# Kernel optimization log

Hardware: AMD Instinct MI355X
Metric: run time of the kernel (lower is better)

Reference implementation:

```python
import jax, jax.numpy as jnp
import numpy as np

D_MODEL = 1024
N_HEADS = 16
D_K = D_MODEL // N_HEADS  # 64
D_V = D_MODEL // N_HEADS  # 64
B, S = 2, 2048


def setup_inputs() -> dict:
    key = jax.random.key(0)
    ks = jax.random.split(key, 8)
    inp = {
        "Q": jax.random.normal(ks[0], (B, S, D_MODEL), dtype=jnp.float32),
        "K": jax.random.normal(ks[1], (B, S, D_MODEL), dtype=jnp.float32),
        "V": jax.random.normal(ks[2], (B, S, D_MODEL), dtype=jnp.float32),
        "prev": jax.random.normal(ks[3], (B, N_HEADS, S, S), dtype=jnp.float32) * 0.1,
        # torch nn.Linear weights are [out_features, in_features]
        "W_Q": jax.random.normal(ks[4], (N_HEADS * D_K, D_MODEL), dtype=jnp.float32) / np.sqrt(D_MODEL),
        "W_K": jax.random.normal(ks[5], (N_HEADS * D_K, D_MODEL), dtype=jnp.float32) / np.sqrt(D_MODEL),
        "W_V": jax.random.normal(ks[6], (N_HEADS * D_V, D_MODEL), dtype=jnp.float32) / np.sqrt(D_MODEL),
        "W_O": jax.random.normal(ks[7], (D_MODEL, N_HEADS * D_V), dtype=jnp.float32) / np.sqrt(N_HEADS * D_V),
    }
    return inp


def reference(Q, K, V, prev, W_Q, W_K, W_V, W_O):
    scale = D_K ** (-0.5)
    # projections: x @ W.T, then split heads -> (b, h, s, d)
    q = jnp.einsum('bsm,em->bse', Q, W_Q).reshape(B, S, N_HEADS, D_K).transpose(0, 2, 1, 3)
    k = jnp.einsum('bsm,em->bse', K, W_K).reshape(B, S, N_HEADS, D_K).transpose(0, 2, 1, 3)
    v = jnp.einsum('bsm,em->bse', V, W_V).reshape(B, S, N_HEADS, D_V).transpose(0, 2, 1, 3)
    scores = jnp.einsum('bhqd,bhkd->bhqk', q, k) * scale + prev
    attn = jax.nn.softmax(scores, axis=-1)  # attn_dropout = 0 (eval)
    context = jnp.einsum('bhqk,bhkd->bhqd', attn, v)
    context = context.transpose(0, 2, 1, 3).reshape(B, S, N_HEADS * D_V)
    output = jnp.einsum('bse,me->bsm', context, W_O)  # proj_dropout = 0 (eval)
    return (output, attn, scores)
```

## Files before the change

### kernel.cpp

```cpp
#include <hip/hip_runtime.h>

#define S_LEN 2048
#define NH 16
#define DH 64
#define DM 1024
#define NB 2
#define BS 4096

typedef __attribute__((ext_vector_type(4))) float f32x4;
typedef __attribute__((ext_vector_type(8))) short bfrag;

__device__ __forceinline__ unsigned short f2bf(float f) {
    unsigned u = __builtin_bit_cast(unsigned, f);
    u += 0x7FFFu + ((u >> 16) & 1u);
    return (unsigned short)(u >> 16);
}

__global__ __launch_bounds__(256) void cast_kernel(const float* __restrict__ in,
                                                   unsigned short* __restrict__ out, int n4) {
    int i = blockIdx.x * 256 + threadIdx.x;
    if (i < n4) {
        float4 v = reinterpret_cast<const float4*>(in)[i];
        ushort4 o;
        o.x = f2bf(v.x); o.y = f2bf(v.y); o.z = f2bf(v.z); o.w = f2bf(v.w);
        reinterpret_cast<ushort4*>(out)[i] = o;
    }
}

template <int EPI>
__global__ __launch_bounds__(256) void gemm_bt(const unsigned short* __restrict__ A,
                                               const unsigned short* __restrict__ Bt,
                                               void* __restrict__ Out, int M, int N, int K) {
    const int tid = threadIdx.x;
    const int lane = tid & 63;
    const int w = tid >> 6, wr = w >> 1, wc = w & 1;
    const int m0 = blockIdx.y * 128;
    const int n0 = blockIdx.x * 128;

    __shared__ unsigned short sA[128 * 64];
    __shared__ unsigned short sB[128 * 64];

    f32x4 acc[4][4];
#pragma unroll
    for (int i = 0; i < 4; ++i)
#pragma unroll
        for (int j = 0; j < 4; ++j) acc[i][j] = (f32x4){0.f, 0.f, 0.f, 0.f};

    for (int k0 = 0; k0 < K; k0 += 64) {
#pragma unroll
        for (int i = 0; i < 4; ++i) {
            int c = i * 256 + tid;
            int row = c >> 3, col8 = c & 7;
            int swz = (col8 * 8) ^ ((row & 7) * 8);
            *reinterpret_cast<int4*>(sA + row * 64 + swz) =
                *reinterpret_cast<const int4*>(A + (size_t)(m0 + row) * K + k0 + col8 * 8);
            *reinterpret_cast<int4*>(sB + row * 64 + swz) =
                *reinterpret_cast<const int4*>(Bt + (size_t)(n0 + row) * K + k0 + col8 * 8);
        }
        __syncthreads();
#pragma unroll
        for (int kk = 0; kk < 2; ++kk) {
            bfrag a[4], b[4];
#pragma unroll
            for (int f = 0; f < 4; ++f) {
                int ra = wr * 64 + f * 16 + (lane & 15);
                a[f] = *reinterpret_cast<const bfrag*>(
                    sA + ra * 64 + ((kk * 32 + (lane >> 4) * 8) ^ ((ra & 7) * 8)));
                int rb = wc * 64 + f * 16 + (lane & 15);
                b[f] = *reinterpret_cast<const bfrag*>(
                    sB + rb * 64 + ((kk * 32 + (lane >> 4) * 8) ^ ((rb & 7) * 8)));
            }
#pragma unroll
            for (int fm = 0; fm < 4; ++fm)
#pragma unroll
                for (int fn = 0; fn < 4; ++fn)
                    acc[fm][fn] =
                        __builtin_amdgcn_mfma_f32_16x16x32_bf16(a[fm], b[fn], acc[fm][fn], 0, 0, 0);
        }
        __syncthreads();
    }

    if constexpr (EPI == 1) {
#pragma unroll
        for (int fm = 0; fm < 4; ++fm)
#pragma unroll
            for (int fn = 0; fn < 4; ++fn) {
                int sbase = m0 + wr * 64 + fm * 16 + ((lane >> 4) << 2);
                int gcol = n0 + wc * 64 + fn * 16 + (lane & 15);
                int b = sbase >> 11, s = sbase & 2047, h = gcol >> 6, d = gcol & 63;
                ushort4 o;
                o.x = f2bf(acc[fm][fn][0]); o.y = f2bf(acc[fm][fn][1]);
                o.z = f2bf(acc[fm][fn][2]); o.w = f2bf(acc[fm][fn][3]);
                *reinterpret_cast<ushort4*>((unsigned short*)Out +
                                            ((size_t)(b * NH + h) * DH + d) * S_LEN + s) = o;
            }
    } else {
#pragma unroll
        for (int fm = 0; fm < 4; ++fm)
#pragma unroll
            for (int fn = 0; fn < 4; ++fn)
#pragma unroll
                for (int r = 0; r < 4; ++r) {
                    int grow = m0 + wr * 64 + fm * 16 + ((lane >> 4) << 2) + r;
                    int gcol = n0 + wc * 64 + fn * 16 + (lane & 15);
                    float v = acc[fm][fn][r];
                    if constexpr (EPI == 0) {
                        int b = grow >> 11, s = grow & 2047, h = gcol >> 6, d = gcol & 63;
                        ((unsigned short*)Out)[((size_t)(b * NH + h) * S_LEN + s) * DH + d] =
                            f2bf(v);
                    } else {
                        ((float*)Out)[(size_t)grow * N + gcol] = v;
                    }
                }
    }
}

__global__ __launch_bounds__(256) void scores_kernel(const unsigned short* __restrict__ qh,
                                                     const unsigned short* __restrict__ kh,
                                                     const float* __restrict__ prev,
                                                     float* __restrict__ scores) {
    const int z = blockIdx.z;
    const int tid = threadIdx.x;
    const int lane = tid & 63;
    const int w = tid >> 6, wr = w >> 1, wc = w & 1;
    const int m0 = blockIdx.y * 128, n0 = blockIdx.x * 128;
    const unsigned short* A = qh + (size_t)z * S_LEN * DH;
    const unsigned short* Bt = kh + (size_t)z * S_LEN * DH;

    __shared__ unsigned short sA[128 * 64];
    __shared__ unsigned short sB[128 * 64];

#pragma unroll
    for (int i = 0; i < 4; ++i) {
        int c = i * 256 + tid;
        int row = c >> 3, col8 = c & 7;
        int swz = (col8 * 8) ^ ((row & 7) * 8);
        *reinterpret_cast<int4*>(sA + row * 64 + swz) =
            *reinterpret_cast<const int4*>(A + (size_t)(m0 + row) * DH + col8 * 8);
        *reinterpret_cast<int4*>(sB + row * 64 + swz) =
            *reinterpret_cast<const int4*>(Bt + (size_t)(n0 + row) * DH + col8 * 8);
    }
    __syncthreads();

    f32x4 acc[4][4];
#pragma unroll
    for (int i = 0; i < 4; ++i)
#pragma unroll
        for (int j = 0; j < 4; ++j) acc[i][j] = (f32x4){0.f, 0.f, 0.f, 0.f};

#pragma unroll
    for (int kk = 0; kk < 2; ++kk) {
        bfrag a[4], b[4];
#pragma unroll
        for (int f = 0; f < 4; ++f) {
            int ra = wr * 64 + f * 16 + (lane & 15);
            a[f] = *reinterpret_cast<const bfrag*>(
                sA + ra * 64 + ((kk * 32 + (lane >> 4) * 8) ^ ((ra & 7) * 8)));
            int rb = wc * 64 + f * 16 + (lane & 15);
            b[f] = *reinterpret_cast<const bfrag*>(
                sB + rb * 64 + ((kk * 32 + (lane >> 4) * 8) ^ ((rb & 7) * 8)));
        }
#pragma unroll
        for (int fm = 0; fm < 4; ++fm)
#pragma unroll
            for (int fn = 0; fn < 4; ++fn)
                acc[fm][fn] =
                    __builtin_amdgcn_mfma_f32_16x16x32_bf16(a[fm], b[fn], acc[fm][fn], 0, 0, 0);
    }

    const float scale = 0.125f;
#pragma unroll
    for (int fm = 0; fm < 4; ++fm)
#pragma unroll
        for (int fn = 0; fn < 4; ++fn)
#pragma unroll
            for (int r = 0; r < 4; ++r) {
                int grow = m0 + wr * 64 + fm * 16 + ((lane >> 4) << 2) + r;
                int gcol = n0 + wc * 64 + fn * 16 + (lane & 15);
                size_t idx = (size_t)z * S_LEN * S_LEN + (size_t)grow * S_LEN + gcol;
                scores[idx] = acc[fm][fn][r] * scale + prev[idx];
            }
}

__global__ __launch_bounds__(256) void softmax_kernel(const float* __restrict__ scores,
                                                      float* __restrict__ attn) {
    const size_t row = (size_t)blockIdx.x * 4 + (threadIdx.x >> 6);
    const int lane = threadIdx.x & 63;
    const float* rp = scores + row * S_LEN;
    float4 v[8];
    float m = -1e30f;
#pragma unroll
    for (int it = 0; it < 8; ++it) {
        v[it] = *reinterpret_cast<const float4*>(rp + (it * 64 + lane) * 4);
        m = fmaxf(m, fmaxf(fmaxf(v[it].x, v[it].y), fmaxf(v[it].z, v[it].w)));
    }
#pragma unroll
    for (int s = 32; s >= 1; s >>= 1) m = fmaxf(m, __shfl_xor(m, s));
    float sum = 0.f;
#pragma unroll
    for (int it = 0; it < 8; ++it) {
        v[it].x = __expf(v[it].x - m); v[it].y = __expf(v[it].y - m);
        v[it].z = __expf(v[it].z - m); v[it].w = __expf(v[it].w - m);
        sum += v[it].x + v[it].y + v[it].z + v[it].w;
    }
#pragma unroll
    for (int s = 32; s >= 1; s >>= 1) sum += __shfl_xor(sum, s);
    const float inv = 1.0f / sum;
    float* op = attn + row * S_LEN;
#pragma unroll
    for (int it = 0; it < 8; ++it) {
        float4 o = make_float4(v[it].x * inv, v[it].y * inv, v[it].z * inv, v[it].w * inv);
        *reinterpret_cast<float4*>(op + (it * 64 + lane) * 4) = o;
    }
}

__global__ __launch_bounds__(256) void pv_kernel(const float* __restrict__ attn,
                                                 const unsigned short* __restrict__ vT,
                                                 unsigned short* __restrict__ ctx) {
    const int z = blockIdx.z;
    const int tid = threadIdx.x, lane = tid & 63;
    const int w = tid >> 6, wr = w >> 1, wc = w & 1;
    const int m0 = blockIdx.x * 128;
    const float* Az = attn + (size_t)z * S_LEN * S_LEN;
    const unsigned short* Bz = vT + (size_t)z * DH * S_LEN;

    __shared__ unsigned short sA[128 * 64];
    __shared__ unsigned short sB[64 * 64];

    f32x4 acc[4][2];
#pragma unroll
    for (int i = 0; i < 4; ++i)
#pragma unroll
        for (int j = 0; j < 2; ++j) acc[i][j] = (f32x4){0.f, 0.f, 0.f, 0.f};

    for (int k0 = 0; k0 < S_LEN; k0 += 64) {
#pragma unroll
        for (int i = 0; i < 8; ++i) {
            int c = i * 256 + tid;
            int row = c >> 4, col4 = c & 15;
            float4 v = *reinterpret_cast<const float4*>(Az + (size_t)(m0 + row) * S_LEN + k0 +
                                                        col4 * 4);
            ushort4 o;
            o.x = f2bf(v.x); o.y = f2bf(v.y); o.z = f2bf(v.z); o.w = f2bf(v.w);
            *reinterpret_cast<ushort4*>(sA + row * 64 + ((col4 * 4) ^ ((row & 7) * 8))) = o;
        }
#pragma unroll
        for (int i = 0; i < 2; ++i) {
            int c = i * 256 + tid;
            int row = c >> 3, col8 = c & 7;
            *reinterpret_cast<int4*>(sB + row * 64 + ((col8 * 8) ^ ((row & 7) * 8))) =
                *reinterpret_cast<const int4*>(Bz + (size_t)row * S_LEN + k0 + col8 * 8);
        }
        __syncthreads();
#pragma unroll
        for (int kk = 0; kk < 2; ++kk) {
            bfrag a[4], b[2];
#pragma unroll
            for (int f = 0; f < 4; ++f) {
                int ra = wr * 64 + f * 16 + (lane & 15);
                a[f] = *reinterpret_cast<const bfrag*>(
                    sA + ra * 64 + ((kk * 32 + (lane >> 4) * 8) ^ ((ra & 7) * 8)));
            }
#pragma unroll
            for (int f = 0; f < 2; ++f) {
                int rb = wc * 32 + f * 16 + (lane & 15);
                b[f] = *reinterpret_cast<const bfrag*>(
                    sB + rb * 64 + ((kk * 32 + (lane >> 4) * 8) ^ ((rb & 7) * 8)));
            }
#pragma unroll
            for (int fm = 0; fm < 4; ++fm)
#pragma unroll
                for (int fn = 0; fn < 2; ++fn)
                    acc[fm][fn] =
                        __builtin_amdgcn_mfma_f32_16x16x32_bf16(a[fm], b[fn], acc[fm][fn], 0, 0, 0);
        }
        __syncthreads();
    }

    const int b = z >> 4, h = z & 15;
#pragma unroll
    for (int fm = 0; fm < 4; ++fm)
#pragma unroll
        for (int fn = 0; fn < 2; ++fn)
#pragma unroll
            for (int r = 0; r < 4; ++r) {
                int s = m0 + wr * 64 + fm * 16 + ((lane >> 4) << 2) + r;
                int d = wc * 32 + fn * 16 + (lane & 15);
                ctx[((size_t)(b * S_LEN + s)) * DM + h * DH + d] = f2bf(acc[fm][fn][r]);
            }
}

extern "C" void kernel_launch(void* const* d_in, const int* in_sizes, int n_in, void* d_out,
                              int out_size, void* d_ws, size_t ws_size, hipStream_t stream) {
    const float* Q = (const float*)d_in[0];
    const float* K = (const float*)d_in[1];
    const float* V = (const float*)d_in[2];
    const float* prev = (const float*)d_in[3];
    const float* Wq = (const float*)d_in[4];
    const float* Wk = (const float*)d_in[5];
    const float* Wv = (const float*)d_in[6];
    const float* Wo = (const float*)d_in[7];

    float* out = (float*)d_out;
    float* attn = out + (size_t)BS * DM;
    float* scores = attn + (size_t)NB * NH * S_LEN * S_LEN;

    unsigned short* ws = (unsigned short*)d_ws;
    unsigned short* Qc = ws;
    unsigned short* Kc = Qc + (size_t)BS * DM;
    unsigned short* Vc = Kc + (size_t)BS * DM;
    unsigned short* Wqc = Vc + (size_t)BS * DM;
    unsigned short* Wkc = Wqc + (size_t)DM * DM;
    unsigned short* Wvc = Wkc + (size_t)DM * DM;
    unsigned short* Woc = Wvc + (size_t)DM * DM;
    unsigned short* qh = Woc + (size_t)DM * DM;
    unsigned short* kh = qh + (size_t)BS * DM;
    unsigned short* vT = kh + (size_t)BS * DM;
    unsigned short* ctx = vT + (size_t)BS * DM;

    cast_kernel<<<BS * DM / 4 / 256, 256, 0, stream>>>(Q, Qc, BS * DM / 4);
    cast_kernel<<<BS * DM / 4 / 256, 256, 0, stream>>>(K, Kc, BS * DM / 4);
    cast_kernel<<<BS * DM / 4 / 256, 256, 0, stream>>>(V, Vc, BS * DM / 4);
    cast_kernel<<<DM * DM / 4 / 256, 256, 0, stream>>>(Wq, Wqc, DM * DM / 4);
    cast_kernel<<<DM * DM / 4 / 256, 256, 0, stream>>>(Wk, Wkc, DM * DM / 4);
    cast_kernel<<<DM * DM / 4 / 256, 256, 0, stream>>>(Wv, Wvc, DM * DM / 4);
    cast_kernel<<<DM * DM / 4 / 256, 256, 0, stream>>>(Wo, Woc, DM * DM / 4);

    dim3 gp(DM / 128, BS / 128, 1);
    gemm_bt<0><<<gp, 256, 0, stream>>>(Qc, Wqc, qh, BS, DM, DM);
    gemm_bt<0><<<gp, 256, 0, stream>>>(Kc, Wkc, kh, BS, DM, DM);
    gemm_bt<1><<<gp, 256, 0, stream>>>(Vc, Wvc, vT, BS, DM, DM);

    dim3 gs(S_LEN / 128, S_LEN / 128, NB * NH);
    scores_kernel<<<gs, 256, 0, stream>>>(qh, kh, prev, scores);

    softmax_kernel<<<NB * NH * S_LEN / 4, 256, 0, stream>>>(scores, attn);

    dim3 gv(S_LEN / 128, 1, NB * NH);
    pv_kernel<<<gv, 256, 0, stream>>>(attn, vT, ctx);

    gemm_bt<2><<<gp, 256, 0, stream>>>(ctx, Woc, out, BS, DM, DM);
}
```

Before: 706.4 us.

## Fuse attention into single two-pass kernel and cast fp32 inputs inside GEMM loads

Replaces the separate scores, softmax and PV kernels with one fused kernel per 128-row query tile. Its first pass computes QK^T plus prev, writes scores and keeps running max and sum. Its second pass rereads scores, writes attn, and feeds bf16 P through shared memory into the PV MFMA. The standalone cast kernels are removed, and the GEMMs now convert fp32 inputs and weights to bf16 while staging tiles into LDS. This aims to cut the full-matrix attn reread by the PV kernel, the separate softmax pass, and several launches. The trade-off is that the fused grid has only 512 blocks with serialized per-block loops, and every GEMM block now repeats the weight conversion.

```diff
diff --git a/kernel.cpp b/kernel.cpp
--- a/kernel.cpp
+++ b/kernel.cpp
@@ -16,20 +16,9 @@
     return (unsigned short)(u >> 16);
 }
 
-__global__ __launch_bounds__(256) void cast_kernel(const float* __restrict__ in,
-                                                   unsigned short* __restrict__ out, int n4) {
-    int i = blockIdx.x * 256 + threadIdx.x;
-    if (i < n4) {
-        float4 v = reinterpret_cast<const float4*>(in)[i];
-        ushort4 o;
-        o.x = f2bf(v.x); o.y = f2bf(v.y); o.z = f2bf(v.z); o.w = f2bf(v.w);
-        reinterpret_cast<ushort4*>(out)[i] = o;
-    }
-}
-
-template <int EPI>
-__global__ __launch_bounds__(256) void gemm_bt(const unsigned short* __restrict__ A,
-                                               const unsigned short* __restrict__ Bt,
+template <int EPI, int AF, int BF>
+__global__ __launch_bounds__(256) void gemm_bt(const void* __restrict__ Av,
+                                               const void* __restrict__ Bv,
                                                void* __restrict__ Out, int M, int N, int K) {
     const int tid = threadIdx.x;
     const int lane = tid & 63;
@@ -47,15 +36,49 @@
         for (int j = 0; j < 4; ++j) acc[i][j] = (f32x4){0.f, 0.f, 0.f, 0.f};
 
     for (int k0 = 0; k0 < K; k0 += 64) {
-#pragma unroll
-        for (int i = 0; i < 4; ++i) {
-            int c = i * 256 + tid;
-            int row = c >> 3, col8 = c & 7;
-            int swz = (col8 * 8) ^ ((row & 7) * 8);
-            *reinterpret_cast<int4*>(sA + row * 64 + swz) =
-                *reinterpret_cast<const int4*>(A + (size_t)(m0 + row) * K + k0 + col8 * 8);
-            *reinterpret_cast<int4*>(sB + row * 64 + swz) =
-                *reinterpret_cast<const int4*>(Bt + (size_t)(n0 + row) * K + k0 + col8 * 8);
+        if constexpr (AF) {
+            const float* A = (const float*)Av;
+#pragma unroll
+            for (int i = 0; i < 8; ++i) {
+                int c = i * 256 + tid;
+                int row = c >> 4, col4 = c & 15;
+                float4 v = *reinterpret_cast<const float4*>(A + (size_t)(m0 + row) * K + k0 +
+                                                            col4 * 4);
+                ushort4 o;
+                o.x = f2bf(v.x); o.y = f2bf(v.y); o.z = f2bf(v.z); o.w = f2bf(v.w);
+                *reinterpret_cast<ushort4*>(sA + row * 64 + ((col4 * 4) ^ ((row & 7) * 8))) = o;
+            }
+        } else {
+            const unsigned short* A = (const unsigned short*)Av;
+#pragma unroll
+            for (int i = 0; i < 4; ++i) {
+                int c = i * 256 + tid;
+                int row = c >> 3, col8 = c & 7;
+                *reinterpret_cast<int4*>(sA + row * 64 + ((col8 * 8) ^ ((row & 7) * 8))) =
+                    *reinterpret_cast<const int4*>(A + (size_t)(m0 + row) * K + k0 + col8 * 8);
+            }
+        }
+        if constexpr (BF) {
+            const float* B = (const float*)Bv;
+#pragma unroll
+            for (int i = 0; i < 8; ++i) {
+                int c = i * 256 + tid;
+                int row = c >> 4, col4 = c & 15;
+                float4 v = *reinterpret_cast<const float4*>(B + (size_t)(n0 + row) * K + k0 +
+                                                            col4 * 4);
+                ushort4 o;
+                o.x = f2bf(v.x); o.y = f2bf(v.y); o.z = f2bf(v.z); o.w = f2bf(v.w);
+                *reinterpret_cast<ushort4*>(sB + row * 64 + ((col4 * 4) ^ ((row & 7) * 8))) = o;
+            }
+        } else {
+            const unsigned short* B = (const unsigned short*)Bv;
+#pragma unroll
+            for (int i = 0; i < 4; ++i) {
+                int c = i * 256 + tid;
+                int row = c >> 3, col8 = c & 7;
+                *reinterpret_cast<int4*>(sB + row * 64 + ((col8 * 8) ^ ((row & 7) * 8))) =
+                    *reinterpret_cast<const int4*>(B + (size_t)(n0 + row) * K + k0 + col8 * 8);
+            }
         }
         __syncthreads();
 #pragma unroll
@@ -115,178 +138,196 @@
     }
 }
 
-__global__ __launch_bounds__(256) void scores_kernel(const unsigned short* __restrict__ qh,
-                                                     const unsigned short* __restrict__ kh,
-                                                     const float* __restrict__ prev,
-                                                     float* __restrict__ scores) {
+__global__ __launch_bounds__(256) void attn_fused(const unsigned short* __restrict__ qh,
+                                                  const unsigned short* __restrict__ kh,
+                                                  const unsigned short* __restrict__ vT,
+                                                  const float* __restrict__ prev,
+                                                  float* __restrict__ scores,
+                                                  float* __restrict__ attn,
+                                                  unsigned short* __restrict__ ctx) {
     const int z = blockIdx.z;
+    const int m0 = blockIdx.x * 128;
     const int tid = threadIdx.x;
     const int lane = tid & 63;
-    const int w = tid >> 6, wr = w >> 1, wc = w & 1;
-    const int m0 = blockIdx.y * 128, n0 = blockIdx.x * 128;
-    const unsigned short* A = qh + (size_t)z * S_LEN * DH;
-    const unsigned short* Bt = kh + (size_t)z * S_LEN * DH;
-
-    __shared__ unsigned short sA[128 * 64];
-    __shared__ unsigned short sB[128 * 64];
+    const int w = tid >> 6;
+
+    __shared__ unsigned short sQ[128 * 64];
+    __shared__ unsigned short sKV[128 * 64];
+    __shared__ unsigned short sP[128 * 128];
+
+    const unsigned short* Qz = qh + (size_t)z * S_LEN * DH;
+    const unsigned short* Kz = kh + (size_t)z * S_LEN * DH;
+    const unsigned short* Vz = vT + (size_t)z * DH * S_LEN;
+    const size_t zbase = (size_t)z * S_LEN * S_LEN;
 
 #pragma unroll
     for (int i = 0; i < 4; ++i) {
         int c = i * 256 + tid;
         int row = c >> 3, col8 = c & 7;
-        int swz = (col8 * 8) ^ ((row & 7) * 8);
-        *reinterpret_cast<int4*>(sA + row * 64 + swz) =
-            *reinterpret_cast<const int4*>(A + (size_t)(m0 + row) * DH + col8 * 8);
-        *reinterpret_cast<int4*>(sB + row * 64 + swz) =
-            *reinterpret_cast<const int4*>(Bt + (size_t)(n0 + row) * DH + col8 * 8);
-    }
-    __syncthreads();
-
-    f32x4 acc[4][4];
-#pragma unroll
-    for (int i = 0; i < 4; ++i)
-#pragma unroll
-        for (int j = 0; j < 4; ++j) acc[i][j] = (f32x4){0.f, 0.f, 0.f, 0.f};
-
-#pragma unroll
-    for (int kk = 0; kk < 2; ++kk) {
-        bfrag a[4], b[4];
-#pragma unroll
-        for (int f = 0; f < 4; ++f) {
-            int ra = wr * 64 + f * 16 + (lane & 15);
-            a[f] = *reinterpret_cast<const bfrag*>(
-                sA + ra * 64 + ((kk * 32 + (lane >> 4) * 8) ^ ((ra & 7) * 8)));
-            int rb = wc * 64 + f * 16 + (lane & 15);
-            b[f] = *reinterpret_cast<const bfrag*>(
-                sB + rb * 64 + ((kk * 32 + (lane >> 4) * 8) ^ ((rb & 7) * 8)));
-        }
-#pragma unroll
-        for (int fm = 0; fm < 4; ++fm)
-#pragma unroll
-            for (int fn = 0; fn < 4; ++fn)
-                acc[fm][fn] =
-                    __builtin_amdgcn_mfma_f32_16x16x32_bf16(a[fm], b[fn], acc[fm][fn], 0, 0, 0);
-    }
+        *reinterpret_cast<int4*>(sQ + row * 64 + ((col8 * 8) ^ ((row & 7) * 8))) =
+            *reinterpret_cast<const int4*>(Qz + (size_t)(m0 + row) * DH + col8 * 8);
+    }
+
+    float m_r[2][4], l_r[2][4];
+#pragma unroll
+    for (int fm = 0; fm < 2; ++fm)
+#pragma unroll
+        for (int r = 0; r < 4; ++r) { m_r[fm][r] = -1e30f; l_r[fm][r] = 0.f; }
 
     const float scale = 0.125f;
-#pragma unroll
-    for (int fm = 0; fm < 4; ++fm)
-#pragma unroll
-        for (int fn = 0; fn < 4; ++fn)
-#pragma unroll
-            for (int r = 0; r < 4; ++r) {
-                int grow = m0 + wr * 64 + fm * 16 + ((lane >> 4) << 2) + r;
-                int gcol = n0 + wc * 64 + fn * 16 + (lane & 15);
-                size_t idx = (size_t)z * S_LEN * S_LEN + (size_t)grow * S_LEN + gcol;
-                scores[idx] = acc[fm][fn][r] * scale + prev[idx];
-            }
-}
-
-__global__ __launch_bounds__(256) void softmax_kernel(const float* __restrict__ scores,
-                                                      float* __restrict__ attn) {
-    const size_t row = (size_t)blockIdx.x * 4 + (threadIdx.x >> 6);
-    const int lane = threadIdx.x & 63;
-    const float* rp = scores + row * S_LEN;
-    float4 v[8];
-    float m = -1e30f;
-#pragma unroll
-    for (int it = 0; it < 8; ++it) {
-        v[it] = *reinterpret_cast<const float4*>(rp + (it * 64 + lane) * 4);
-        m = fmaxf(m, fmaxf(fmaxf(v[it].x, v[it].y), fmaxf(v[it].z, v[it].w)));
-    }
-#pragma unroll
-    for (int s = 32; s >= 1; s >>= 1) m = fmaxf(m, __shfl_xor(m, s));
-    float sum = 0.f;
-#pragma unroll
-    for (int it = 0; it < 8; ++it) {
-        v[it].x = __expf(v[it].x - m); v[it].y = __expf(v[it].y - m);
-        v[it].z = __expf(v[it].z - m); v[it].w = __expf(v[it].w - m);
-        sum += v[it].x + v[it].y + v[it].z + v[it].w;
-    }
-#pragma unroll
-    for (int s = 32; s >= 1; s >>= 1) sum += __shfl_xor(sum, s);
-    const float inv = 1.0f / sum;
-    float* op = attn + row * S_LEN;
-#pragma unroll
-    for (int it = 0; it < 8; ++it) {
-        float4 o = make_float4(v[it].x * inv, v[it].y * inv, v[it].z * inv, v[it].w * inv);
-        *reinterpret_cast<float4*>(op + (it * 64 + lane) * 4) = o;
-    }
-}
-
-__global__ __launch_bounds__(256) void pv_kernel(const float* __restrict__ attn,
-                                                 const unsigned short* __restrict__ vT,
-                                                 unsigned short* __restrict__ ctx) {
-    const int z = blockIdx.z;
-    const int tid = threadIdx.x, lane = tid & 63;
-    const int w = tid >> 6, wr = w >> 1, wc = w & 1;
-    const int m0 = blockIdx.x * 128;
-    const float* Az = attn + (size_t)z * S_LEN * S_LEN;
-    const unsigned short* Bz = vT + (size_t)z * DH * S_LEN;
-
-    __shared__ unsigned short sA[128 * 64];
-    __shared__ unsigned short sB[64 * 64];
-
-    f32x4 acc[4][2];
-#pragma unroll
-    for (int i = 0; i < 4; ++i)
-#pragma unroll
-        for (int j = 0; j < 2; ++j) acc[i][j] = (f32x4){0.f, 0.f, 0.f, 0.f};
-
-    for (int k0 = 0; k0 < S_LEN; k0 += 64) {
-#pragma unroll
-        for (int i = 0; i < 8; ++i) {
-            int c = i * 256 + tid;
-            int row = c >> 4, col4 = c & 15;
-            float4 v = *reinterpret_cast<const float4*>(Az + (size_t)(m0 + row) * S_LEN + k0 +
-                                                        col4 * 4);
-            ushort4 o;
-            o.x = f2bf(v.x); o.y = f2bf(v.y); o.z = f2bf(v.z); o.w = f2bf(v.w);
-            *reinterpret_cast<ushort4*>(sA + row * 64 + ((col4 * 4) ^ ((row & 7) * 8))) = o;
-        }
-#pragma unroll
-        for (int i = 0; i < 2; ++i) {
+
+    for (int kt = 0; kt < S_LEN / 128; ++kt) {
+        const int n0 = kt * 128;
+        __syncthreads();
+#pragma unroll
+        for (int i = 0; i < 4; ++i) {
             int c = i * 256 + tid;
             int row = c >> 3, col8 = c & 7;
-            *reinterpret_cast<int4*>(sB + row * 64 + ((col8 * 8) ^ ((row & 7) * 8))) =
-                *reinterpret_cast<const int4*>(Bz + (size_t)row * S_LEN + k0 + col8 * 8);
-        }
-        __syncthreads();
+            *reinterpret_cast<int4*>(sKV + row * 64 + ((col8 * 8) ^ ((row & 7) * 8))) =
+                *reinterpret_cast<const int4*>(Kz + (size_t)(n0 + row) * DH + col8 * 8);
+        }
+        __syncthreads();
+
+        f32x4 acc[2][8];
+#pragma unroll
+        for (int fm = 0; fm < 2; ++fm)
+#pragma unroll
+            for (int fn = 0; fn < 8; ++fn) acc[fm][fn] = (f32x4){0.f, 0.f, 0.f, 0.f};
+
 #pragma unroll
         for (int kk = 0; kk < 2; ++kk) {
-            bfrag a[4], b[2];
-#pragma unroll
-            for (int f = 0; f < 4; ++f) {
-                int ra = wr * 64 + f * 16 + (lane & 15);
+            bfrag a[2], b[8];
+#pragma unroll
+            for (int f = 0; f < 2; ++f) {
+                int ra = w * 32 + f * 16 + (lane & 15);
                 a[f] = *reinterpret_cast<const bfrag*>(
-                    sA + ra * 64 + ((kk * 32 + (lane >> 4) * 8) ^ ((ra & 7) * 8)));
-            }
-#pragma unroll
-            for (int f = 0; f < 2; ++f) {
-                int rb = wc * 32 + f * 16 + (lane & 15);
+                    sQ + ra * 64 + ((kk * 32 + (lane >> 4) * 8) ^ ((ra & 7) * 8)));
+            }
+#pragma unroll
+            for (int f = 0; f < 8; ++f) {
+                int rb = f * 16 + (lane & 15);
                 b[f] = *reinterpret_cast<const bfrag*>(
-                    sB + rb * 64 + ((kk * 32 + (lane >> 4) * 8) ^ ((rb & 7) * 8)));
-            }
-#pragma unroll
-            for (int fm = 0; fm < 4; ++fm)
-#pragma unroll
-                for (int fn = 0; fn < 2; ++fn)
+                    sKV + rb * 64 + ((kk * 32 + (lane >> 4) * 8) ^ ((rb & 7) * 8)));
+            }
+#pragma unroll
+            for (int fm = 0; fm < 2; ++fm)
+#pragma unroll
+                for (int fn = 0; fn < 8; ++fn)
                     acc[fm][fn] =
                         __builtin_amdgcn_mfma_f32_16x16x32_bf16(a[fm], b[fn], acc[fm][fn], 0, 0, 0);
         }
-        __syncthreads();
+
+#pragma unroll
+        for (int fm = 0; fm < 2; ++fm) {
+            const int growb = m0 + w * 32 + fm * 16 + ((lane >> 4) << 2);
+#pragma unroll
+            for (int fn = 0; fn < 8; ++fn) {
+                const int gcol = n0 + fn * 16 + (lane & 15);
+#pragma unroll
+                for (int r = 0; r < 4; ++r) {
+                    size_t idx = zbase + (size_t)(growb + r) * S_LEN + gcol;
+                    float s = acc[fm][fn][r] * scale + prev[idx];
+                    scores[idx] = s;
+                    acc[fm][fn][r] = s;
+                }
+            }
+#pragma unroll
+            for (int r = 0; r < 4; ++r) {
+                float pm = acc[fm][0][r];
+#pragma unroll
+                for (int fn = 1; fn < 8; ++fn) pm = fmaxf(pm, acc[fm][fn][r]);
+                pm = fmaxf(pm, __shfl_xor(pm, 1));
+                pm = fmaxf(pm, __shfl_xor(pm, 2));
+                pm = fmaxf(pm, __shfl_xor(pm, 4));
+                pm = fmaxf(pm, __shfl_xor(pm, 8));
+                float mnew = fmaxf(m_r[fm][r], pm);
+                float psum = 0.f;
+#pragma unroll
+                for (int fn = 0; fn < 8; ++fn) psum += __expf(acc[fm][fn][r] - mnew);
+                psum += __shfl_xor(psum, 1);
+                psum += __shfl_xor(psum, 2);
+                psum += __shfl_xor(psum, 4);
+                psum += __shfl_xor(psum, 8);
+                l_r[fm][r] = l_r[fm][r] * __expf(m_r[fm][r] - mnew) + psum;
+                m_r[fm][r] = mnew;
+            }
+        }
+    }
+
+    float inv_l[2][4];
+#pragma unroll
+    for (int fm = 0; fm < 2; ++fm)
+#pragma unroll
+        for (int r = 0; r < 4; ++r) inv_l[fm][r] = 1.0f / l_r[fm][r];
+
+    f32x4 acco[2][4];
+#pragma unroll
+    for (int fm = 0; fm < 2; ++fm)
+#pragma unroll
+        for (int fn = 0; fn < 4; ++fn) acco[fm][fn] = (f32x4){0.f, 0.f, 0.f, 0.f};
+
+    for (int kt = 0; kt < S_LEN / 128; ++kt) {
+        const int n0 = kt * 128;
+        __syncthreads();
+#pragma unroll
+        for (int i = 0; i < 4; ++i) {
+            int c = i * 256 + tid;
+            int row = c >> 4, col8 = c & 15;
+            *reinterpret_cast<int4*>(sKV + row * 128 + (((col8 ^ (row & 7)) << 3))) =
+                *reinterpret_cast<const int4*>(Vz + (size_t)row * S_LEN + n0 + col8 * 8);
+        }
+#pragma unroll
+        for (int fm = 0; fm < 2; ++fm) {
+            const int prowb = w * 32 + fm * 16 + ((lane >> 4) << 2);
+#pragma unroll
+            for (int fn = 0; fn < 8; ++fn) {
+                const int pcol = fn * 16 + (lane & 15);
+#pragma unroll
+                for (int r = 0; r < 4; ++r) {
+                    size_t idx = zbase + (size_t)(m0 + prowb + r) * S_LEN + n0 + pcol;
+                    float s = scores[idx];
+                    float p = __expf(s - m_r[fm][r]) * inv_l[fm][r];
+                    attn[idx] = p;
+                    sP[(prowb + r) * 128 + ((((pcol >> 3) ^ ((prowb + r) & 7)) << 3)) +
+                       (pcol & 7)] = f2bf(p);
+                }
+            }
+        }
+        __syncthreads();
+#pragma unroll
+        for (int kk = 0; kk < 4; ++kk) {
+            bfrag a[2], b[4];
+#pragma unroll
+            for (int f = 0; f < 2; ++f) {
+                int ra = w * 32 + f * 16 + (lane & 15);
+                a[f] = *reinterpret_cast<const bfrag*>(
+                    sP + ra * 128 + (((kk * 4 + (lane >> 4)) ^ (ra & 7)) << 3));
+            }
+#pragma unroll
+            for (int f = 0; f < 4; ++f) {
+                int rb = f * 16 + (lane & 15);
+                b[f] = *reinterpret_cast<const bfrag*>(
+                    sKV + rb * 128 + (((kk * 4 + (lane >> 4)) ^ (rb & 7)) << 3));
+            }
+#pragma unroll
+            for (int fm = 0; fm < 2; ++fm)
+#pragma unroll
+                for (int fn = 0; fn < 4; ++fn)
+                    acco[fm][fn] =
+                        __builtin_amdgcn_mfma_f32_16x16x32_bf16(a[fm], b[fn], acco[fm][fn], 0, 0, 0);
+        }
     }
 
     const int b = z >> 4, h = z & 15;
 #pragma unroll
-    for (int fm = 0; fm < 4; ++fm)
-#pragma unroll
-        for (int fn = 0; fn < 2; ++fn)
+    for (int fm = 0; fm < 2; ++fm)
+#pragma unroll
+        for (int fn = 0; fn < 4; ++fn)
 #pragma unroll
             for (int r = 0; r < 4; ++r) {
-                int s = m0 + wr * 64 + fm * 16 + ((lane >> 4) << 2) + r;
-                int d = wc * 32 + fn * 16 + (lane & 15);
-                ctx[((size_t)(b * S_LEN + s)) * DM + h * DH + d] = f2bf(acc[fm][fn][r]);
+                int s = m0 + w * 32 + fm * 16 + ((lane >> 4) << 2) + r;
+                int d = fn * 16 + (lane & 15);
+                ctx[((size_t)(b * S_LEN + s)) * DM + h * DH + d] = f2bf(acco[fm][fn][r]);
             }
 }
 
@@ -306,38 +347,18 @@
     float* scores = attn + (size_t)NB * NH * S_LEN * S_LEN;
 
     unsigned short* ws = (unsigned short*)d_ws;
-    unsigned short* Qc = ws;
-    unsigned short* Kc = Qc + (size_t)BS * DM;
-    unsigned short* Vc = Kc + (size_t)BS * DM;
-    unsigned short* Wqc = Vc + (size_t)BS * DM;
-    unsigned short* Wkc = Wqc + (size_t)DM * DM;
-    unsigned short* Wvc = Wkc + (size_t)DM * DM;
-    unsigned short* Woc = Wvc + (size_t)DM * DM;
-    unsigned short* qh = Woc + (size_t)DM * DM;
+    unsigned short* qh = ws;
     unsigned short* kh = qh + (size_t)BS * DM;
     unsigned short* vT = kh + (size_t)BS * DM;
     unsigned short* ctx = vT + (size_t)BS * DM;
 
-    cast_kernel<<<BS * DM / 4 / 256, 256, 0, stream>>>(Q, Qc, BS * DM / 4);
-    cast_kernel<<<BS * DM / 4 / 256, 256, 0, stream>>>(K, Kc, BS * DM / 4);
-    cast_kernel<<<BS * DM / 4 / 256, 256, 0, stream>>>(V, Vc, BS * DM / 4);
-    cast_kernel<<<DM * DM / 4 / 256, 256, 0, stream>>>(Wq, Wqc, DM * DM / 4);
-    cast_kernel<<<DM * DM / 4 / 256, 256, 0, stream>>>(Wk, Wkc, DM * DM / 4);
-    cast_kernel<<<DM * DM / 4 / 256, 256, 0, stream>>>(Wv, Wvc, DM * DM / 4);
-    cast_kernel<<<DM * DM / 4 / 256, 256, 0, stream>>>(Wo, Woc, DM * DM / 4);
-
     dim3 gp(DM / 128, BS / 128, 1);
-    gemm_bt<0><<<gp, 256, 0, stream>>>(Qc, Wqc, qh, BS, DM, DM);
-    gemm_bt<0><<<gp, 256, 0, stream>>>(Kc, Wkc, kh, BS, DM, DM);
-    gemm_bt<1><<<gp, 256, 0, stream>>>(Vc, Wvc, vT, BS, DM, DM);
-
-    dim3 gs(S_LEN / 128, S_LEN / 128, NB * NH);
-    scores_kernel<<<gs, 256, 0, stream>>>(qh, kh, prev, scores);
-
-    softmax_kernel<<<NB * NH * S_LEN / 4, 256, 0, stream>>>(scores, attn);
-
-    dim3 gv(S_LEN / 128, 1, NB * NH);
-    pv_kernel<<<gv, 256, 0, stream>>>(attn, vT, ctx);
-
-    gemm_bt<2><<<gp, 256, 0, stream>>>(ctx, Woc, out, BS, DM, DM);
+    gemm_bt<0, 1, 1><<<gp, 256, 0, stream>>>(Q, Wq, qh, BS, DM, DM);
+    gemm_bt<0, 1, 1><<<gp, 256, 0, stream>>>(K, Wk, kh, BS, DM, DM);
+    gemm_bt<1, 1, 1><<<gp, 256, 0, stream>>>(V, Wv, vT, BS, DM, DM);
+
+    dim3 ga(S_LEN / 128, 1, NB * NH);
+    attn_fused<<<ga, 256, 0, stream>>>(qh, kh, vT, prev, scores, attn, ctx);
+
+    gemm_bt<2, 0, 1><<<gp, 256, 0, stream>>>(ctx, Wo, out, BS, DM, DM);
 }
```

Result: slower. 1.283 ms (+81.7%).
